# Kernel tuning notes

Hardware: AMD Instinct MI355X
Metric: run time of the kernel (lower is better)

Reference implementation:

```python
import jax, jax.numpy as jnp
import numpy as np

B, N, F_IN, F_OUT = 4, 2048, 256, 128
ALPHA = 0.2  # LeakyReLU negative slope
EPS = 1e-5   # LayerNorm eps
NEG = -9e15


def setup_inputs() -> dict:
    key = jax.random.key(0)
    k1, k2, k3, k4 = jax.random.split(key, 4)
    h = jax.random.normal(k1, (B, N, F_IN), dtype=jnp.float32)
    adj = jax.random.randint(k2, (B, N, N), 0, 2, dtype=jnp.int32)
    # xavier_uniform with gain=1.414 for W
    limW = 1.414 * np.sqrt(6.0 / (F_IN + F_OUT))
    W = jax.random.uniform(k3, (F_IN, F_OUT), dtype=jnp.float32, minval=-limW, maxval=limW)
    # kaiming_uniform (leaky_relu, a=alpha, fan_in=2*F_OUT) for a
    gain = np.sqrt(2.0 / (1.0 + ALPHA ** 2))
    lima = gain * np.sqrt(3.0 / (2 * F_OUT))
    a = jax.random.uniform(k4, (2 * F_OUT, 1), dtype=jnp.float32, minval=-lima, maxval=lima)
    gamma = jnp.ones((F_OUT,), dtype=jnp.float32)
    beta = jnp.zeros((F_OUT,), dtype=jnp.float32)
    return {"h": h, "adj": adj, "W": W, "a": a, "gamma": gamma, "beta": beta}


def reference(h, adj, W, a, gamma, beta):
    Wh = jnp.einsum("bnf,fo->bno", h, W)            # [B,N,F_out]
    a1, a2 = a[:F_OUT, 0], a[F_OUT:, 0]              # [F_out] each
    s1 = Wh @ a1                                      # [B,N] score of node i
    s2 = Wh @ a2                                      # [B,N] score of node j
    # e[b,i,j] = LeakyReLU(s1[b,i] + s2[b,j])  -- avoids O(N^2*2F) concat tensor
    e = s1[:, :, None] + s2[:, None, :]
    e = jnp.where(e >= 0, e, ALPHA * e)
    e = jnp.where(adj > 0, e, NEG)
    attention = jax.nn.softmax(e, axis=2)             # [B,N,N]
    h_prime = jnp.einsum("bij,bjo->bio", attention, Wh)
    mu = jnp.mean(h_prime, axis=-1, keepdims=True)
    var = jnp.var(h_prime, axis=-1, keepdims=True)
    h_norm = (h_prime - mu) / jnp.sqrt(var + EPS) * gamma + beta
    return jax.nn.gelu(h_norm, approximate=False)
```

## Files before the change

### kernel.cpp

```cpp
#include <hip/hip_runtime.h>
#include <hip/hip_bf16.h>

typedef __attribute__((ext_vector_type(8))) short bf16x8;
typedef __attribute__((ext_vector_type(4))) float f32x4;

#define NB   4
#define NN   2048
#define FIN  256
#define FOUT 128
#define SPLIT 4
#define JCH  (NN / SPLIT)
#define NSTEP (JCH / 64)

__device__ __forceinline__ unsigned short f2bf(float f) {
    unsigned int u = __builtin_bit_cast(unsigned int, f);
    u += 0x7fffu + ((u >> 16) & 1u);
    return (unsigned short)(u >> 16);
}
__device__ __forceinline__ float bf2f(unsigned short s) {
    return __builtin_bit_cast(float, (unsigned int)s << 16);
}

__global__ __launch_bounds__(256) void k_wt(const float* __restrict__ W,
                                            unsigned short* __restrict__ WT) {
    int idx = blockIdx.x * 256 + threadIdx.x;
    int k = idx & 255, o = idx >> 8;
    WT[idx] = f2bf(W[k * FOUT + o]);
}

__global__ __launch_bounds__(256) void k_wh(const float* __restrict__ h,
                                            const float* __restrict__ a,
                                            const unsigned short* __restrict__ WT,
                                            unsigned short* __restrict__ WhB,
                                            float* __restrict__ s1,
                                            float* __restrict__ s2) {
    __shared__ unsigned short hs[16][264];
    __shared__ float s1w[4][16], s2w[4][16];
    int t = threadIdx.x, blk = blockIdx.x;
    int nglob0 = blk * 16;
    int b = nglob0 >> 11;

    const float4* h4 = (const float4*)h + (size_t)blk * 1024;
    #pragma unroll
    for (int i = 0; i < 4; ++i) {
        int idx = i * 256 + t;
        float4 v = h4[idx];
        int row = idx >> 6, c4 = (idx & 63) * 4;
        unsigned int lo = (unsigned int)f2bf(v.x) | ((unsigned int)f2bf(v.y) << 16);
        unsigned int hi = (unsigned int)f2bf(v.z) | ((unsigned int)f2bf(v.w) << 16);
        *(uint2*)&hs[row][c4] = make_uint2(lo, hi);
    }
    __syncthreads();

    int w = t >> 6, l = t & 63, lr = l & 15, lk = l >> 4;
    float a1v[2], a2v[2];
    #pragma unroll
    for (int j = 0; j < 2; ++j) {
        a1v[j] = a[(w * 2 + j) * 16 + lr];
        a2v[j] = a[FOUT + (w * 2 + j) * 16 + lr];
    }
    f32x4 acc[2] = {{0.f,0.f,0.f,0.f},{0.f,0.f,0.f,0.f}};

    #pragma unroll
    for (int kk = 0; kk < 8; ++kk) {
        int k0 = kk * 32;
        bf16x8 af = *(const bf16x8*)&hs[lr][k0 + lk * 8];
        #pragma unroll
        for (int j = 0; j < 2; ++j) {
            bf16x8 bfr = *(const bf16x8*)(WT + ((w * 2 + j) * 16 + lr) * 256 + k0 + lk * 8);
            acc[j] = __builtin_amdgcn_mfma_f32_16x16x32_bf16(af, bfr, acc[j], 0, 0, 0);
        }
    }

    int n0 = nglob0 & 2047;
    int sIdx = n0 >> 6;
    int hh   = (n0 >> 5) & 1;
    int bklo = (n0 & 31) >> 3;
    float v1[4] = {0.f,0.f,0.f,0.f}, v2[4] = {0.f,0.f,0.f,0.f};
    #pragma unroll
    for (int j = 0; j < 2; ++j) {
        int ot = w * 2 + j;
        float x0 = acc[j][0], x1 = acc[j][1], x2 = acc[j][2], x3 = acc[j][3];
        ushort4 pk;
        pk.x = f2bf(x0); pk.y = f2bf(x1); pk.z = f2bf(x2); pk.w = f2bf(x3);
        size_t fragBase = (((size_t)(b * 8 + ot) * 32 + sIdx) * 2 + hh) * 64;
        size_t lane = fragBase + lr + 16 * (bklo + (lk >> 1));
        *(ushort4*)(WhB + lane * 8 + (lk & 1) * 4) = pk;
        v1[0] += x0 * a1v[j]; v1[1] += x1 * a1v[j]; v1[2] += x2 * a1v[j]; v1[3] += x3 * a1v[j];
        v2[0] += x0 * a2v[j]; v2[1] += x1 * a2v[j]; v2[2] += x2 * a2v[j]; v2[3] += x3 * a2v[j];
    }
    #pragma unroll
    for (int m = 1; m < 16; m <<= 1)
        #pragma unroll
        for (int r = 0; r < 4; ++r) {
            v1[r] += __shfl_xor(v1[r], m);
            v2[r] += __shfl_xor(v2[r], m);
        }
    if (lr == 0)
        #pragma unroll
        for (int r = 0; r < 4; ++r) {
            s1w[w][lk * 4 + r] = v1[r];
            s2w[w][lk * 4 + r] = v2[r];
        }
    __syncthreads();
    if (t < 16) {
        s1[nglob0 + t] = s1w[0][t] + s1w[1][t] + s1w[2][t] + s1w[3][t];
        s2[nglob0 + t] = s2w[0][t] + s2w[1][t] + s2w[2][t] + s2w[3][t];
    }
}

__global__ __launch_bounds__(256) void k_attn(const int* __restrict__ adj,
                                              const unsigned short* __restrict__ WhB,
                                              const float* __restrict__ s1,
                                              const float* __restrict__ s2,
                                              unsigned short* __restrict__ num,
                                              float* __restrict__ Zp) {
    __shared__ union {
        unsigned short Ps[2][64][72];
        float hS[64][132];
        unsigned char sc[4][2048];
    } S;
    __shared__ unsigned int nibS[64][20];
    __shared__ float s2S[JCH];

    int t = threadIdx.x, w = t >> 6, l = t & 63, lr = l & 15, lk = l >> 4;
    int bid = blockIdx.x;
    int bi = (bid >> 3) + (bid & 7) * 64;
    int part = bi >> 7, rem = bi & 127;
    int b = rem >> 5, i0 = (rem & 31) * 64, j0 = part * JCH;

    {
        unsigned char* sh = S.sc[w];
        const int* aBase = adj + ((size_t)(b * NN) + i0 + w * 16) * NN + j0;
        #pragma unroll
        for (int batch = 0; batch < 4; ++batch) {
            int4 v[4][2];
            #pragma unroll
            for (int r = 0; r < 4; ++r) {
                const int* rp = aBase + (size_t)(batch * 4 + r) * NN + l * 8;
                v[r][0] = *(const int4*)rp;
                v[r][1] = *(const int4*)(rp + 4);
            }
            #pragma unroll
            for (int r = 0; r < 4; ++r) {
                unsigned char b0 = (unsigned char)((v[r][0].x > 0) | ((v[r][0].y > 0) << 1) |
                                                   ((v[r][0].z > 0) << 2) | ((v[r][0].w > 0) << 3));
                unsigned char b1 = (unsigned char)((v[r][1].x > 0) | ((v[r][1].y > 0) << 1) |
                                                   ((v[r][1].z > 0) << 2) | ((v[r][1].w > 0) << 3));
                sh[(batch * 4 + r) * 128 + l * 2]     = b0;
                sh[(batch * 4 + r) * 128 + l * 2 + 1] = b1;
            }
        }
        asm volatile("s_waitcnt lgkmcnt(0)" ::: "memory");
        #pragma unroll
        for (int q = 0; q < 4; ++q) {
            int d = q * 64 + l;
            int row = d >> 4, c = d & 15;
            uint2 u = *(const uint2*)&sh[row * 128 + c * 8];
            unsigned int lo = (u.x & 0xFu) | ((u.x >> 4) & 0xF0u) |
                              ((u.x >> 8) & 0xF00u) | ((u.x >> 12) & 0xF000u);
            unsigned int hi = (u.y & 0xFu) | ((u.y >> 4) & 0xF0u) |
                              ((u.y >> 8) & 0xF00u) | ((u.y >> 12) & 0xF000u);
            nibS[w * 16 + row][c] = lo | (hi << 16);
        }
        if (t < 128) ((float4*)s2S)[t] = ((const float4*)(s2 + b * NN + j0))[t];
    }
    float s1r = s1[b * NN + i0 + w * 16 + lr];

    const unsigned short* B0 = WhB + (((size_t)(b * 8 + w * 2) * 32 + part * NSTEP) * 2) * 512 + (size_t)l * 8;
    const unsigned short* B1 = B0 + (size_t)32 * 2 * 512;
    bf16x8 bB[2][2][2];
    #pragma unroll
    for (int s = 0; s < 2; ++s) {
        bB[s][0][0] = *(const bf16x8*)(B0 + s * 1024);
        bB[s][0][1] = *(const bf16x8*)(B0 + s * 1024 + 512);
        bB[s][1][0] = *(const bf16x8*)(B1 + s * 1024);
        bB[s][1][1] = *(const bf16x8*)(B1 + s * 1024 + 512);
    }

    f32x4 acc[4][2];
    #pragma unroll
    for (int rg = 0; rg < 4; ++rg) {
        acc[rg][0] = (f32x4){0.f,0.f,0.f,0.f};
        acc[rg][1] = (f32x4){0.f,0.f,0.f,0.f};
    }
    float zacc = 0.f;

    __syncthreads();

    #pragma unroll
    for (int s = 0; s < NSTEP; ++s) {
        const int slot = s & 1;
        {
            unsigned int word = nibS[w * 16 + lr][s * 2 + (lk >> 1)] >> ((lk & 1) * 16);
            const float* sp = &s2S[s * 64 + lk * 16];
            float4 f0 = *(const float4*)sp,       f1 = *(const float4*)(sp + 4);
            float4 f2 = *(const float4*)(sp + 8), f3 = *(const float4*)(sp + 12);
            float sv[16] = {f0.x,f0.y,f0.z,f0.w, f1.x,f1.y,f1.z,f1.w,
                            f2.x,f2.y,f2.z,f2.w, f3.x,f3.y,f3.z,f3.w};
            unsigned int pw[8];
            #pragma unroll
            for (int q = 0; q < 8; ++q) {
                float e0 = s1r + sv[2 * q];
                float e1 = s1r + sv[2 * q + 1];
                e0 = fmaxf(e0, 0.2f * e0);
                e1 = fmaxf(e1, 0.2f * e1);
                float p0 = ((word >> (2 * q))     & 1u) ? __expf(e0) : 0.f;
                float p1 = ((word >> (2 * q + 1)) & 1u) ? __expf(e1) : 0.f;
                zacc += p0 + p1;
                pw[q] = (unsigned int)f2bf(p0) | ((unsigned int)f2bf(p1) << 16);
            }
            *(uint4*)&S.Ps[slot][w * 16 + lr][lk * 16]     = (uint4){pw[0], pw[1], pw[2], pw[3]};
            *(uint4*)&S.Ps[slot][w * 16 + lr][lk * 16 + 8] = (uint4){pw[4], pw[5], pw[6], pw[7]};
        }
        asm volatile("s_waitcnt lgkmcnt(0)" ::: "memory");
        __builtin_amdgcn_s_barrier();
        __builtin_amdgcn_sched_barrier(0);

        bf16x8 c00 = bB[slot][0][0], c01 = bB[slot][0][1];
        bf16x8 c10 = bB[slot][1][0], c11 = bB[slot][1][1];
        if (s < NSTEP - 2) {
            bB[slot][0][0] = *(const bf16x8*)(B0 + (s + 2) * 1024);
            bB[slot][0][1] = *(const bf16x8*)(B0 + (s + 2) * 1024 + 512);
            bB[slot][1][0] = *(const bf16x8*)(B1 + (s + 2) * 1024);
            bB[slot][1][1] = *(const bf16x8*)(B1 + (s + 2) * 1024 + 512);
        }

        #pragma unroll
        for (int rg = 0; rg < 4; ++rg) {
            bf16x8 a0 = *(const bf16x8*)&S.Ps[slot][rg * 16 + lr][lk * 8];
            bf16x8 a1 = *(const bf16x8*)&S.Ps[slot][rg * 16 + lr][32 + lk * 8];
            acc[rg][0] = __builtin_amdgcn_mfma_f32_16x16x32_bf16(a0, c00, acc[rg][0], 0, 0, 0);
            acc[rg][0] = __builtin_amdgcn_mfma_f32_16x16x32_bf16(a1, c01, acc[rg][0], 0, 0, 0);
            acc[rg][1] = __builtin_amdgcn_mfma_f32_16x16x32_bf16(a0, c10, acc[rg][1], 0, 0, 0);
            acc[rg][1] = __builtin_amdgcn_mfma_f32_16x16x32_bf16(a1, c11, acc[rg][1], 0, 0, 0);
        }
    }

    zacc += __shfl_xor(zacc, 16);
    zacc += __shfl_xor(zacc, 32);
    if (l < 16) Zp[(size_t)(part * NB + b) * NN + i0 + w * 16 + l] = zacc;

    __syncthreads();
    #pragma unroll
    for (int rg = 0; rg < 4; ++rg)
        #pragma unroll
        for (int ot2 = 0; ot2 < 2; ++ot2)
            #pragma unroll
            for (int r = 0; r < 4; ++r)
                S.hS[rg * 16 + lk * 4 + r][(w * 2 + ot2) * 16 + lr] = acc[rg][ot2][r];
    __syncthreads();

    unsigned short* np = num + ((size_t)(part * NB + b) * NN + i0) * FOUT;
    #pragma unroll
    for (int q = 0; q < 4; ++q) {
        int flat = q * 256 + t;
        int row = flat >> 4, c8 = (flat & 15) * 8;
        float4 v0 = *(const float4*)&S.hS[row][c8];
        float4 v1 = *(const float4*)&S.hS[row][c8 + 4];
        uint4 pk;
        pk.x = (unsigned int)f2bf(v0.x) | ((unsigned int)f2bf(v0.y) << 16);
        pk.y = (unsigned int)f2bf(v0.z) | ((unsigned int)f2bf(v0.w) << 16);
        pk.z = (unsigned int)f2bf(v1.x) | ((unsigned int)f2bf(v1.y) << 16);
        pk.w = (unsigned int)f2bf(v1.z) | ((unsigned int)f2bf(v1.w) << 16);
        *(uint4*)(np + (size_t)row * FOUT + c8) = pk;
    }
}

__global__ __launch_bounds__(256) void k_final(const unsigned short* __restrict__ num,
                                               const float* __restrict__ Zp,
                                               const float* __restrict__ gamma,
                                               const float* __restrict__ beta,
                                               float* __restrict__ out) {
    int t = threadIdx.x, bi = blockIdx.x;
    int rowA = t >> 5;
    int c0 = (t & 31) * 4;
    size_t gn = (size_t)bi * 8 + rowA;
    int b = (int)(gn >> 11), n = (int)(gn & 2047);

    float Z = 0.f;
    #pragma unroll
    for (int p = 0; p < SPLIT; ++p) Z += Zp[(size_t)(p * NB + b) * NN + n];

    float x[4] = {0.f, 0.f, 0.f, 0.f};
    #pragma unroll
    for (int p = 0; p < SPLIT; ++p) {
        const unsigned short* np = num + ((size_t)(p * NB + b) * NN + n) * FOUT + c0;
        ushort4 u = *(const ushort4*)np;
        x[0] += bf2f(u.x); x[1] += bf2f(u.y); x[2] += bf2f(u.z); x[3] += bf2f(u.w);
    }
    float rz = 1.f / Z;
    #pragma unroll
    for (int i = 0; i < 4; ++i) x[i] *= rz;

    float sm = 0.f, sq = 0.f;
    #pragma unroll
    for (int i = 0; i < 4; ++i) { sm += x[i]; sq += x[i] * x[i]; }
    #pragma unroll
    for (int m = 1; m < 32; m <<= 1) {
        sm += __shfl_xor(sm, m);
        sq += __shfl_xor(sq, m);
    }
    float mu  = sm * (1.f / 128.f);
    float var = sq * (1.f / 128.f) - mu * mu;
    float rs  = rsqrtf(var + 1e-5f);
    float4 g0 = *(const float4*)(gamma + c0);
    float4 e0 = *(const float4*)(beta + c0);
    float gg[4] = {g0.x, g0.y, g0.z, g0.w};
    float bb[4] = {e0.x, e0.y, e0.z, e0.w};
    float y[4];
    #pragma unroll
    for (int i = 0; i < 4; ++i) {
        float v = (x[i] - mu) * rs * gg[i] + bb[i];
        y[i] = 0.5f * v * (1.f + erff(v * 0.70710678118f));
    }
    float* op = out + gn * FOUT + c0;
    *(float4*)op = make_float4(y[0], y[1], y[2], y[3]);
}

extern "C" void kernel_launch(void* const* d_in, const int* in_sizes, int n_in,
                              void* d_out, int out_size, void* d_ws, size_t ws_size,
                              hipStream_t stream) {
    const float* h     = (const float*)d_in[0];
    const int*   adj   = (const int*)d_in[1];
    const float* W     = (const float*)d_in[2];
    const float* a     = (const float*)d_in[3];
    const float* gamma = (const float*)d_in[4];
    const float* beta  = (const float*)d_in[5];
    float* out = (float*)d_out;

    char* ws = (char*)d_ws;
    unsigned short* WT  = (unsigned short*)ws;
    unsigned short* WhB = (unsigned short*)(ws + (1u << 16));
    float* s1 = (float*)(ws + 2162688);
    float* s2 = (float*)(ws + 2195456);
    float* Zp = (float*)(ws + 2228224);
    unsigned short* num = (unsigned short*)(ws + 2359296);

    hipLaunchKernelGGL(k_wt,    dim3(128),  dim3(256), 0, stream, W, WT);
    hipLaunchKernelGGL(k_wh,    dim3(512),  dim3(256), 0, stream, h, a, WT, WhB, s1, s2);
    hipLaunchKernelGGL(k_attn,  dim3(512),  dim3(256), 0, stream, adj, WhB, s1, s2, num, Zp);
    hipLaunchKernelGGL(k_final, dim3(1024), dim3(256), 0, stream, num, Zp, gamma, beta, out);
}
```

Baseline: 46.70 us.

## Stream adjacency mask per step from global memory instead of LDS nibble prepass

Removes the upfront prepass that loaded the whole adjacency tile, packed it into bitmasks in shared memory and then repacked it into nibbles. Each lane now loads its own 16 adjacency ints per step straight from global memory, double-buffered two steps ahead in registers alongside the existing Wh prefetch, and tests them directly. This is meant to overlap the adjacency reads with the softmax/MFMA loop and cut LDS usage and the prologue latency. It costs more registers and less coalesced 64-byte row segments per lane. The Ps padding also changes from 72 to 76.

New measurement: 39.56 us, median of 2. 1.18x faster.

```diff
diff --git a/kernel.cpp b/kernel.cpp
--- a/kernel.cpp
+++ b/kernel.cpp
@@ -116,11 +116,9 @@
                                               unsigned short* __restrict__ num,
                                               float* __restrict__ Zp) {
     __shared__ union {
-        unsigned short Ps[2][64][72];
+        unsigned short Ps[2][64][76];
         float hS[64][132];
-        unsigned char sc[4][2048];
     } S;
-    __shared__ unsigned int nibS[64][20];
     __shared__ float s2S[JCH];
 
     int t = threadIdx.x, w = t >> 6, l = t & 63, lr = l & 15, lk = l >> 4;
@@ -129,43 +127,16 @@
     int part = bi >> 7, rem = bi & 127;
     int b = rem >> 5, i0 = (rem & 31) * 64, j0 = part * JCH;
 
-    {
-        unsigned char* sh = S.sc[w];
-        const int* aBase = adj + ((size_t)(b * NN) + i0 + w * 16) * NN + j0;
-        #pragma unroll
-        for (int batch = 0; batch < 4; ++batch) {
-            int4 v[4][2];
-            #pragma unroll
-            for (int r = 0; r < 4; ++r) {
-                const int* rp = aBase + (size_t)(batch * 4 + r) * NN + l * 8;
-                v[r][0] = *(const int4*)rp;
-                v[r][1] = *(const int4*)(rp + 4);
-            }
-            #pragma unroll
-            for (int r = 0; r < 4; ++r) {
-                unsigned char b0 = (unsigned char)((v[r][0].x > 0) | ((v[r][0].y > 0) << 1) |
-                                                   ((v[r][0].z > 0) << 2) | ((v[r][0].w > 0) << 3));
-                unsigned char b1 = (unsigned char)((v[r][1].x > 0) | ((v[r][1].y > 0) << 1) |
-                                                   ((v[r][1].z > 0) << 2) | ((v[r][1].w > 0) << 3));
-                sh[(batch * 4 + r) * 128 + l * 2]     = b0;
-                sh[(batch * 4 + r) * 128 + l * 2 + 1] = b1;
-            }
-        }
-        asm volatile("s_waitcnt lgkmcnt(0)" ::: "memory");
-        #pragma unroll
-        for (int q = 0; q < 4; ++q) {
-            int d = q * 64 + l;
-            int row = d >> 4, c = d & 15;
-            uint2 u = *(const uint2*)&sh[row * 128 + c * 8];
-            unsigned int lo = (u.x & 0xFu) | ((u.x >> 4) & 0xF0u) |
-                              ((u.x >> 8) & 0xF00u) | ((u.x >> 12) & 0xF000u);
-            unsigned int hi = (u.y & 0xFu) | ((u.y >> 4) & 0xF0u) |
-                              ((u.y >> 8) & 0xF00u) | ((u.y >> 12) & 0xF000u);
-            nibS[w * 16 + row][c] = lo | (hi << 16);
-        }
-        if (t < 128) ((float4*)s2S)[t] = ((const float4*)(s2 + b * NN + j0))[t];
-    }
+    if (t < 128) ((float4*)s2S)[t] = ((const float4*)(s2 + b * NN + j0))[t];
     float s1r = s1[b * NN + i0 + w * 16 + lr];
+
+    const int* aRow = adj + ((size_t)(b * NN) + i0 + w * 16 + lr) * NN + j0 + lk * 16;
+    int4 av[2][4];
+    #pragma unroll
+    for (int s = 0; s < 2; ++s)
+        #pragma unroll
+        for (int q = 0; q < 4; ++q)
+            av[s][q] = *(const int4*)(aRow + s * 64 + q * 4);
 
     const unsigned short* B0 = WhB + (((size_t)(b * 8 + w * 2) * 32 + part * NSTEP) * 2) * 512 + (size_t)l * 8;
     const unsigned short* B1 = B0 + (size_t)32 * 2 * 512;
@@ -191,8 +162,16 @@
     #pragma unroll
     for (int s = 0; s < NSTEP; ++s) {
         const int slot = s & 1;
+        int4 m0 = av[slot][0], m1 = av[slot][1], m2 = av[slot][2], m3 = av[slot][3];
+        if (s < NSTEP - 2) {
+            #pragma unroll
+            for (int q = 0; q < 4; ++q)
+                av[slot][q] = *(const int4*)(aRow + (s + 2) * 64 + q * 4);
+        }
+
         {
-            unsigned int word = nibS[w * 16 + lr][s * 2 + (lk >> 1)] >> ((lk & 1) * 16);
+            int mv[16] = {m0.x, m0.y, m0.z, m0.w, m1.x, m1.y, m1.z, m1.w,
+                          m2.x, m2.y, m2.z, m2.w, m3.x, m3.y, m3.z, m3.w};
             const float* sp = &s2S[s * 64 + lk * 16];
             float4 f0 = *(const float4*)sp,       f1 = *(const float4*)(sp + 4);
             float4 f2 = *(const float4*)(sp + 8), f3 = *(const float4*)(sp + 12);
@@ -205,8 +184,8 @@
                 float e1 = s1r + sv[2 * q + 1];
                 e0 = fmaxf(e0, 0.2f * e0);
                 e1 = fmaxf(e1, 0.2f * e1);
-                float p0 = ((word >> (2 * q))     & 1u) ? __expf(e0) : 0.f;
-                float p1 = ((word >> (2 * q + 1)) & 1u) ? __expf(e1) : 0.f;
+                float p0 = (mv[2 * q]     > 0) ? __expf(e0) : 0.f;
+                float p1 = (mv[2 * q + 1] > 0) ? __expf(e1) : 0.f;
                 zacc += p0 + p1;
                 pw[q] = (unsigned int)f2bf(p0) | ((unsigned int)f2bf(p1) << 16);
             }
```
